# Performance work log

Hardware: AMD Instinct MI355X
Metric: run time of the kernel (lower is better)

Reference implementation:

```python
import jax, jax.numpy as jnp
import numpy as np

D_MODEL = 1024
NHEAD = 16
D_K = D_MODEL // NHEAD
D_CHUNK = 128


def setup_inputs() -> dict:
    key = jax.random.key(0)
    ks = jax.random.split(key, 11)
    B, S = 4, 8192
    s = 1.0 / np.sqrt(D_MODEL)
    inp = {
        "q": jax.random.normal(ks[0], (B, S, D_MODEL), jnp.float32),
        "k": jax.random.normal(ks[1], (B, S, D_MODEL), jnp.float32),
        "v": jax.random.normal(ks[2], (B, S, D_MODEL), jnp.float32),
        "W_Q": jax.random.normal(ks[3], (D_MODEL, D_MODEL), jnp.float32) * s,
        "b_Q": jnp.zeros((D_MODEL,), jnp.float32),
        "W_K": jax.random.normal(ks[4], (D_MODEL, D_MODEL), jnp.float32) * s,
        "b_K": jnp.zeros((D_MODEL,), jnp.float32),
        "W_V": jax.random.normal(ks[5], (D_MODEL, D_MODEL), jnp.float32) * s,
        "b_V": jnp.zeros((D_MODEL,), jnp.float32),
        "W_O": jax.random.normal(ks[6], (D_MODEL, D_MODEL), jnp.float32) * s,
        "b_O": jnp.zeros((D_MODEL,), jnp.float32),
    }
    return inp


def reference(q, k, v, W_Q, b_Q, W_K, b_K, W_V, b_V, W_O, b_O):
    B, S, _ = q.shape
    C = S // D_CHUNK  # number of chunks

    def split_heads(x):
        # [B,S,D] -> [B,H,C,P,dk]  (matches view+transpose+view in torch)
        x = x.reshape(B, S, NHEAD, D_K).transpose(0, 2, 1, 3)
        return x.reshape(B, NHEAD, C, D_CHUNK, D_K)

    Q = split_heads(q @ W_Q.T + b_Q)
    K = split_heads(k @ W_K.T + b_K)
    V = split_heads(v @ W_V.T + b_V)

    # block-diagonal local attention: each [P,P] score matrix per (b,h,chunk)
    scores = jnp.einsum("bhcpd,bhcqd->bhcpq", Q, K) / np.sqrt(D_K).astype(jnp.float32)
    attn_w = jax.nn.softmax(scores, axis=-1)
    attn = jnp.einsum("bhcpq,bhcqd->bhcpd", attn_w, V)  # [B,H,C,P,dk]

    # Faithful to torch: attn.transpose(1,2).view(B,-1,d_model)
    # i.e. flatten [C,H,P,dk] contiguously into rows of d_model.
    concat = attn.transpose(0, 2, 1, 3, 4).reshape(B, S, D_MODEL)
    return concat @ W_O.T + b_O
```

## Files before the change

kernel.cpp:

```cpp
#include <hip/hip_runtime.h>
#include <hip/hip_bf16.h>


typedef __attribute__((ext_vector_type(8))) short short8;
typedef __attribute__((ext_vector_type(4))) float f32x4;
typedef __attribute__((ext_vector_type(4))) unsigned short us4;
typedef __attribute__((ext_vector_type(4))) unsigned int u32x4;
typedef __attribute__((ext_vector_type(2))) unsigned int u32x2;

__device__ __forceinline__ unsigned short f2bf(float f) {
  unsigned u = __float_as_uint(f);
  u += 0x7fffu + ((u >> 16) & 1u);
  return (unsigned short)(u >> 16);
}

__device__ __forceinline__ unsigned cvtpk(float lo, float hi) {
  unsigned r;
  asm("v_cvt_pk_bf16_f32 %0, %1, %2" : "=v"(r) : "v"(lo), "v"(hi));
  return r;
}

__device__ __forceinline__ void gload16(const void* g, void* l) {
  __builtin_amdgcn_global_load_lds((const __attribute__((address_space(1))) void*)g,
                                   (__attribute__((address_space(3))) void*)l, 16, 0, 0);
}

__global__ void f2b4_kernel(const float* __restrict__ i0, const float* __restrict__ i1,
                            const float* __restrict__ i2, const float* __restrict__ i3,
                            unsigned short* __restrict__ o0, unsigned short* __restrict__ o1,
                            unsigned short* __restrict__ o2, unsigned short* __restrict__ o3,
                            int n) {
  const int z = blockIdx.z;
  const float* in = z == 0 ? i0 : z == 1 ? i1 : z == 2 ? i2 : i3;
  unsigned short* out = z == 0 ? o0 : z == 1 ? o1 : z == 2 ? o2 : o3;
  int i = (blockIdx.x * 256 + threadIdx.x) * 4;
  if (i >= n) return;
  f32x4 x = *(const f32x4*)(in + i);
  u32x2 o;
  o[0] = cvtpk(x[0], x[1]);
  o[1] = cvtpk(x[2], x[3]);
  *(u32x2*)(out + i) = o;
}

template<bool A_F32, bool C_F32>
__device__ __forceinline__ void gemm_core(const void* __restrict__ Apv,
                                          const unsigned short* __restrict__ Bp,
                                          const float* __restrict__ bias,
                                          void* __restrict__ Cp) {
  constexpr int BK = 64, NT = 16;
  const int tid = threadIdx.x;
  const int lane = tid & 63, wave = tid >> 6;
  const int lg = lane >> 4, li = lane & 15;
  const int wr = wave >> 2, wc = wave & 3;

  const unsigned short* Ab = (const unsigned short*)Apv;
  const float* Af = (const float*)Apv;

  const int orig = blockIdx.y * 4 + blockIdx.x;
  const int wg = (orig & 7) * 64 + (orig >> 3);
  const int bn = wg & 3, bm = wg >> 2;

  const long arow0 = (long)bm * 256;
  const int bcol0 = bn * 256;

  __shared__ __align__(16) unsigned short As[2][256 * BK];
  __shared__ __align__(16) unsigned short Bs[2][256 * BK];

  float bv[4];
  #pragma unroll
  for (int n = 0; n < 4; ++n) bv[n] = bias[bcol0 + wc * 64 + n * 16 + li];

  f32x4 acc[8][4];
  #pragma unroll
  for (int m = 0; m < 8; ++m)
    #pragma unroll
    for (int n = 0; n < 4; ++n) acc[m][n] = (f32x4){0.f, 0.f, 0.f, 0.f};

  auto stage_half = [&](int u, int h) {
    const int k0 = u * BK;
    const int half = h & 1;
    unsigned short* dst = (h < 2 ? As[u & 1] : Bs[u & 1]) + half * (128 * BK);
    const unsigned short* src = (h < 2) ? Ab : Bp;
    const long rbase = (h < 2) ? (arow0 + half * 128) : (long)(bcol0 + half * 128);
    #pragma unroll
    for (int it = 0; it < 2; ++it) {
      int s = it * 512 + tid;
      int row = s >> 3;
      int eg = ((s & 7) ^ (row & 7)) * 8;
      gload16(src + (rbase + row) * 1024 + k0 + eg, (unsigned char*)dst + s * 16);
    }
  };

  f32x4 areg[4][2];
  auto issueA = [&](int u) {
    #pragma unroll
    for (int hf = 0; hf < 2; ++hf)
      #pragma unroll
      for (int it = 0; it < 2; ++it) {
        int s = it * 512 + tid;
        int row = s >> 3;
        int ce = ((s & 7) ^ (row & 7)) * 8;
        const float* p = Af + (arow0 + hf * 128 + row) * 1024 + u * BK + ce;
        areg[hf * 2 + it][0] = *(const f32x4*)p;
        areg[hf * 2 + it][1] = *(const f32x4*)(p + 4);
      }
  };
  auto writeA_half = [&](int u, int hf) {
    unsigned short* dstb = As[u & 1] + hf * (128 * BK);
    #pragma unroll
    for (int it = 0; it < 2; ++it) {
      int s = it * 512 + tid;
      u32x4 o;
      o[0] = cvtpk(areg[hf * 2 + it][0][0], areg[hf * 2 + it][0][1]);
      o[1] = cvtpk(areg[hf * 2 + it][0][2], areg[hf * 2 + it][0][3]);
      o[2] = cvtpk(areg[hf * 2 + it][1][0], areg[hf * 2 + it][1][1]);
      o[3] = cvtpk(areg[hf * 2 + it][1][2], areg[hf * 2 + it][1][3]);
      *(u32x4*)((unsigned char*)dstb + s * 16) = o;
    }
  };

  if constexpr (A_F32) {
    stage_half(0, 2); stage_half(0, 3);
    issueA(0);
    stage_half(1, 2); stage_half(1, 3);
    writeA_half(0, 0); writeA_half(0, 1);
    asm volatile("s_waitcnt lgkmcnt(0)" ::: "memory");
    __builtin_amdgcn_sched_barrier(0);
    __builtin_amdgcn_s_barrier();
  } else {
    stage_half(0, 0); stage_half(0, 1); stage_half(0, 2); stage_half(0, 3);
    stage_half(1, 2); stage_half(1, 3);
    asm volatile("s_waitcnt vmcnt(4)" ::: "memory");
    __builtin_amdgcn_sched_barrier(0);
    __builtin_amdgcn_s_barrier();
  }

  for (int t = 0; t < NT; ++t) {
    const unsigned short* Asb = As[t & 1];
    const unsigned short* Bsb = Bs[t & 1];

    auto LDA = [&](int m, int kk) {
      return *(const short8*)(Asb + (wr * 128 + m * 16 + li) * BK +
                              (((kk * 4 + lg) ^ (li & 7)) * 8));
    };
    auto LDB = [&](int n, int kk) {
      return *(const short8*)(Bsb + (wc * 64 + n * 16 + li) * BK +
                              (((kk * 4 + lg) ^ (li & 7)) * 8));
    };

    short8 b0[4], b1[4];

    {
      short8 a0[4];
      #pragma unroll
      for (int i = 0; i < 4; ++i) a0[i] = LDA(i, 0);
      #pragma unroll
      for (int n = 0; n < 4; ++n) b0[n] = LDB(n, 0);
      if constexpr (A_F32) {
        if (t + 1 < NT) issueA(t + 1);
      } else {
        if (t + 1 < NT) stage_half(t + 1, 0);
      }
      __builtin_amdgcn_s_barrier();
      __builtin_amdgcn_s_setprio(1);
      #pragma unroll
      for (int i = 0; i < 4; ++i)
        #pragma unroll
        for (int n = 0; n < 4; ++n)
          acc[i][n] = __builtin_amdgcn_mfma_f32_16x16x32_bf16(a0[i], b0[n], acc[i][n], 0, 0, 0);
      __builtin_amdgcn_s_setprio(0);
      __builtin_amdgcn_s_barrier();
    }
    {
      short8 a1[4];
      #pragma unroll
      for (int i = 0; i < 4; ++i) a1[i] = LDA(i, 1);
      #pragma unroll
      for (int n = 0; n < 4; ++n) b1[n] = LDB(n, 1);
      if constexpr (!A_F32) {
        if (t + 1 < NT) stage_half(t + 1, 1);
      }
      __builtin_amdgcn_s_barrier();
      __builtin_amdgcn_s_setprio(1);
      #pragma unroll
      for (int i = 0; i < 4; ++i)
        #pragma unroll
        for (int n = 0; n < 4; ++n)
          acc[i][n] = __builtin_amdgcn_mfma_f32_16x16x32_bf16(a1[i], b1[n], acc[i][n], 0, 0, 0);
      __builtin_amdgcn_s_setprio(0);
      __builtin_amdgcn_s_barrier();
    }
    {
      short8 a2[4];
      #pragma unroll
      for (int i = 0; i < 4; ++i) a2[i] = LDA(4 + i, 0);
      if (t + 2 < NT) stage_half(t + 2, 2);
      __builtin_amdgcn_s_barrier();
      __builtin_amdgcn_s_setprio(1);
      #pragma unroll
      for (int i = 0; i < 4; ++i)
        #pragma unroll
        for (int n = 0; n < 4; ++n)
          acc[4 + i][n] = __builtin_amdgcn_mfma_f32_16x16x32_bf16(a2[i], b0[n], acc[4 + i][n], 0, 0, 0);
      if constexpr (A_F32) {
        if (t + 1 < NT) writeA_half(t + 1, 0);
      }
      __builtin_amdgcn_s_setprio(0);
      __builtin_amdgcn_s_barrier();
    }
    {
      short8 a3[4];
      #pragma unroll
      for (int i = 0; i < 4; ++i) a3[i] = LDA(4 + i, 1);
      if (t + 2 < NT) stage_half(t + 2, 3);
      if constexpr (!A_F32) {
        if (t + 2 < NT) {
          asm volatile("s_waitcnt vmcnt(4)" ::: "memory");
        } else {
          asm volatile("s_waitcnt vmcnt(0)" ::: "memory");
        }
        __builtin_amdgcn_sched_barrier(0);
      }
      __builtin_amdgcn_s_barrier();
      __builtin_amdgcn_s_setprio(1);
      #pragma unroll
      for (int i = 0; i < 4; ++i)
        #pragma unroll
        for (int n = 0; n < 4; ++n)
          acc[4 + i][n] = __builtin_amdgcn_mfma_f32_16x16x32_bf16(a3[i], b1[n], acc[4 + i][n], 0, 0, 0);
      if constexpr (A_F32) {
        if (t + 1 < NT) writeA_half(t + 1, 1);
        asm volatile("s_waitcnt lgkmcnt(0)" ::: "memory");
        __builtin_amdgcn_sched_barrier(0);
      }
      __builtin_amdgcn_s_setprio(0);
      __builtin_amdgcn_s_barrier();
    }
  }

  float* wsc = (float*)As + wave * (16 * 68);
  #pragma unroll
  for (int m = 0; m < 8; ++m) {
    #pragma unroll
    for (int n = 0; n < 4; ++n)
      #pragma unroll
      for (int r = 0; r < 4; ++r)
        wsc[(lg * 4 + r) * 68 + n * 16 + li] = acc[m][n][r] + bv[n];
    asm volatile("s_waitcnt lgkmcnt(0)" ::: "memory");
    __builtin_amdgcn_sched_barrier(0);
    #pragma unroll
    for (int i = 0; i < 4; ++i) {
      int slot = i * 64 + lane;
      int r = slot >> 4, g = slot & 15;
      f32x4 vv = *(const f32x4*)(wsc + r * 68 + g * 4);
      long grow = arow0 + wr * 128 + m * 16 + r;
      long gcol = bcol0 + wc * 64 + g * 4;
      if constexpr (C_F32) {
        *(f32x4*)((float*)Cp + grow * 1024 + gcol) = vv;
      } else {
        u32x2 o;
        o[0] = cvtpk(vv[0], vv[1]);
        o[1] = cvtpk(vv[2], vv[3]);
        *(u32x2*)((unsigned short*)Cp + grow * 1024 + gcol) = o;
      }
    }
    asm volatile("s_waitcnt lgkmcnt(0)" ::: "memory");
    __builtin_amdgcn_sched_barrier(0);
  }
}

__global__ __launch_bounds__(512, 2)
void gemm_proj(const float* __restrict__ A0, const float* __restrict__ A1,
               const float* __restrict__ A2,
               const unsigned short* __restrict__ B0, const unsigned short* __restrict__ B1,
               const unsigned short* __restrict__ B2,
               const float* __restrict__ b0, const float* __restrict__ b1,
               const float* __restrict__ b2,
               unsigned short* __restrict__ C0, unsigned short* __restrict__ C1,
               unsigned short* __restrict__ C2) {
  const int z = blockIdx.z;
  const float* Ap          = z == 0 ? A0 : z == 1 ? A1 : A2;
  const unsigned short* Bp = z == 0 ? B0 : z == 1 ? B1 : B2;
  const float* bias        = z == 0 ? b0 : z == 1 ? b1 : b2;
  unsigned short* Cp       = z == 0 ? C0 : z == 1 ? C1 : C2;
  gemm_core<true, false>(Ap, Bp, bias, Cp);
}

__global__ __launch_bounds__(512, 2)
void gemm_out(const unsigned short* __restrict__ Ap, const unsigned short* __restrict__ Bp,
              const float* __restrict__ bias, float* __restrict__ Cp) {
  gemm_core<false, true>(Ap, Bp, bias, Cp);
}

__global__ __launch_bounds__(256)
void attn_kernel(const unsigned short* __restrict__ Qp, const unsigned short* __restrict__ Kp,
                 const unsigned short* __restrict__ Vp, unsigned short* __restrict__ Cc) {
  const int bid = blockIdx.x;
  const int c = bid & 63, h = (bid >> 6) & 15, b = bid >> 10;
  const int tid = threadIdx.x;
  const int lane = tid & 63, wave = tid >> 6;
  const int lg = lane >> 4, li = lane & 15;

  __shared__ __align__(16) unsigned short Qs[128 * 64];
  __shared__ __align__(16) unsigned short Ks[128 * 64];
  __shared__ __align__(16) unsigned short Vs[128 * 64];
  __shared__ __align__(16) unsigned short Ps[4][32 * 128];

  const long base = ((long)(b * 8192 + c * 128)) * 1024 + h * 64;
  #pragma unroll
  for (int it = 0; it < 4; ++it) {
    int slot = it * 256 + tid;
    int row = slot >> 3;
    int colsw = ((slot & 7) ^ (row & 7)) * 8;
    int collin = (slot & 7) * 8;
    gload16(Qp + base + (long)row * 1024 + colsw, (unsigned char*)Qs + slot * 16);
    gload16(Kp + base + (long)row * 1024 + colsw, (unsigned char*)Ks + slot * 16);
    gload16(Vp + base + (long)row * 1024 + collin, (unsigned char*)Vs + slot * 16);
  }
  __syncthreads();

  f32x4 sc[2][8];
  #pragma unroll
  for (int m = 0; m < 2; ++m)
    #pragma unroll
    for (int n = 0; n < 8; ++n) sc[m][n] = (f32x4){0.f, 0.f, 0.f, 0.f};

  short8 qf[2][2];
  #pragma unroll
  for (int m = 0; m < 2; ++m)
    #pragma unroll
    for (int ks = 0; ks < 2; ++ks)
      qf[m][ks] = *(const short8*)(Qs + (wave * 32 + m * 16 + li) * 64 +
                                   (((ks * 4 + lg) ^ (li & 7)) * 8));

  #pragma unroll
  for (int n = 0; n < 8; ++n) {
    short8 kf0 = *(const short8*)(Ks + (n * 16 + li) * 64 + ((lg ^ (li & 7)) * 8));
    short8 kf1 = *(const short8*)(Ks + (n * 16 + li) * 64 + (((4 + lg) ^ (li & 7)) * 8));
    #pragma unroll
    for (int m = 0; m < 2; ++m) {
      sc[m][n] = __builtin_amdgcn_mfma_f32_16x16x32_bf16(qf[m][0], kf0, sc[m][n], 0, 0, 0);
      sc[m][n] = __builtin_amdgcn_mfma_f32_16x16x32_bf16(qf[m][1], kf1, sc[m][n], 0, 0, 0);
    }
  }

  #pragma unroll
  for (int m = 0; m < 2; ++m)
    #pragma unroll
    for (int r = 0; r < 4; ++r) {
      float mx = sc[m][0][r];
      #pragma unroll
      for (int n = 1; n < 8; ++n) mx = fmaxf(mx, sc[m][n][r]);
      #pragma unroll
      for (int d = 1; d < 16; d <<= 1) mx = fmaxf(mx, __shfl_xor(mx, d));
      float sum = 0.f;
      #pragma unroll
      for (int n = 0; n < 8; ++n) {
        float p = __expf((sc[m][n][r] - mx) * 0.125f);
        sc[m][n][r] = p;
        sum += p;
      }
      #pragma unroll
      for (int d = 1; d < 16; d <<= 1) sum += __shfl_xor(sum, d);
      float rinv = 1.f / sum;
      #pragma unroll
      for (int n = 0; n < 8; ++n) sc[m][n][r] *= rinv;
    }

  #pragma unroll
  for (int m = 0; m < 2; ++m)
    #pragma unroll
    for (int n = 0; n < 8; ++n)
      #pragma unroll
      for (int r = 0; r < 4; ++r) {
        int row = m * 16 + lg * 4 + r;
        int col = n * 16 + li;
        Ps[wave][row * 128 + (((col >> 3) ^ (row & 7)) * 8) + (col & 7)] = f2bf(sc[m][n][r]);
      }
  __syncthreads();

  f32x4 oc[2][4];
  #pragma unroll
  for (int m = 0; m < 2; ++m)
    #pragma unroll
    for (int n = 0; n < 4; ++n) oc[m][n] = (f32x4){0.f, 0.f, 0.f, 0.f};

  #pragma unroll
  for (int ks = 0; ks < 4; ++ks) {
    short8 vf[4];
    #pragma unroll
    for (int n = 0; n < 4; ++n)
      #pragma unroll
      for (int j = 0; j < 8; ++j)
        vf[n][j] = (short)Vs[(ks * 32 + lg * 8 + j) * 64 + n * 16 + li];
    #pragma unroll
    for (int m = 0; m < 2; ++m) {
      short8 pf = *(const short8*)(Ps[wave] + (m * 16 + li) * 128 +
                                   (((ks * 4 + lg) ^ (li & 7)) * 8));
      #pragma unroll
      for (int n = 0; n < 4; ++n)
        oc[m][n] = __builtin_amdgcn_mfma_f32_16x16x32_bf16(pf, vf[n], oc[m][n], 0, 0, 0);
    }
  }

  #pragma unroll
  for (int m = 0; m < 2; ++m)
    #pragma unroll
    for (int n = 0; n < 4; ++n)
      #pragma unroll
      for (int r = 0; r < 4; ++r) {
        int p = wave * 32 + m * 16 + lg * 4 + r;
        int d = n * 16 + li;
        int s = c * 128 + h * 8 + (p >> 4);
        int colo = (p & 15) * 64 + d;
        Cc[((long)(b * 8192 + s)) * 1024 + colo] = f2bf(oc[m][n][r]);
      }
}

extern "C" void kernel_launch(void* const* d_in, const int* in_sizes, int n_in,
                              void* d_out, int out_size, void* d_ws, size_t ws_size,
                              hipStream_t stream) {
  (void)in_sizes; (void)n_in; (void)out_size; (void)ws_size;
  const float* q  = (const float*)d_in[0];
  const float* k  = (const float*)d_in[1];
  const float* v  = (const float*)d_in[2];
  const float* WQ = (const float*)d_in[3];
  const float* bQ = (const float*)d_in[4];
  const float* WK = (const float*)d_in[5];
  const float* bK = (const float*)d_in[6];
  const float* WV = (const float*)d_in[7];
  const float* bV = (const float*)d_in[8];
  const float* WO = (const float*)d_in[9];
  const float* bO = (const float*)d_in[10];

  const size_t MN = 32768ull * 1024ull;
  unsigned short* Qp  = (unsigned short*)d_ws;
  unsigned short* Kp  = Qp + MN;
  unsigned short* Vp  = Kp + MN;
  unsigned short* Cc  = Vp + MN;
  unsigned short* WQb = Cc + MN;
  unsigned short* WKb = WQb + (1 << 20);
  unsigned short* WVb = WKb + (1 << 20);
  unsigned short* WOb = WVb + (1 << 20);

  dim3 gw(1024, 1, 4);
  f2b4_kernel<<<gw, 256, 0, stream>>>(WQ, WK, WV, WO, WQb, WKb, WVb, WOb, 1 << 20);

  dim3 gp(4, 128, 3);
  gemm_proj<<<gp, 512, 0, stream>>>(q, k, v, WQb, WKb, WVb, bQ, bK, bV, Qp, Kp, Vp);

  attn_kernel<<<4096, 256, 0, stream>>>(Qp, Kp, Vp, Cc);

  dim3 go(4, 128);
  gemm_out<<<go, 512, 0, stream>>>(Cc, WOb, bO, (float*)d_out);
}
```

Baseline: 514.2 us.

## Prefetch fp32 A tiles two steps ahead with ping-pong register buffers

For the fp32-A GEMM path, the global loads of the A tile are now issued two k-iterations ahead instead of one, using two alternating register buffers (even and odd). The main loop is unrolled by two so the buffers swap roles statically, and explicit vmcnt waits gate the convert-and-write to LDS. The aim is to hide more global-load latency for the fp32 activations. In exchange it doubles the A staging registers, which risks lower occupancy or spills, and the loop assumes NT is even.

```diff
diff --git a/kernel.cpp b/kernel.cpp
--- a/kernel.cpp
+++ b/kernel.cpp
@@ -91,8 +91,8 @@
     }
   };
 
-  f32x4 areg[4][2];
-  auto issueA = [&](int u) {
+  f32x4 aregE[4][2], aregO[4][2];
+  auto issueA = [&](int u, f32x4 (&ar)[4][2]) {
     #pragma unroll
     for (int hf = 0; hf < 2; ++hf)
       #pragma unroll
@@ -101,29 +101,143 @@
         int row = s >> 3;
         int ce = ((s & 7) ^ (row & 7)) * 8;
         const float* p = Af + (arow0 + hf * 128 + row) * 1024 + u * BK + ce;
-        areg[hf * 2 + it][0] = *(const f32x4*)p;
-        areg[hf * 2 + it][1] = *(const f32x4*)(p + 4);
+        ar[hf * 2 + it][0] = *(const f32x4*)p;
+        ar[hf * 2 + it][1] = *(const f32x4*)(p + 4);
       }
   };
-  auto writeA_half = [&](int u, int hf) {
+  auto writeAh = [&](int u, int hf, f32x4 (&ar)[4][2]) {
     unsigned short* dstb = As[u & 1] + hf * (128 * BK);
     #pragma unroll
     for (int it = 0; it < 2; ++it) {
       int s = it * 512 + tid;
       u32x4 o;
-      o[0] = cvtpk(areg[hf * 2 + it][0][0], areg[hf * 2 + it][0][1]);
-      o[1] = cvtpk(areg[hf * 2 + it][0][2], areg[hf * 2 + it][0][3]);
-      o[2] = cvtpk(areg[hf * 2 + it][1][0], areg[hf * 2 + it][1][1]);
-      o[3] = cvtpk(areg[hf * 2 + it][1][2], areg[hf * 2 + it][1][3]);
+      o[0] = cvtpk(ar[hf * 2 + it][0][0], ar[hf * 2 + it][0][1]);
+      o[1] = cvtpk(ar[hf * 2 + it][0][2], ar[hf * 2 + it][0][3]);
+      o[2] = cvtpk(ar[hf * 2 + it][1][0], ar[hf * 2 + it][1][1]);
+      o[3] = cvtpk(ar[hf * 2 + it][1][2], ar[hf * 2 + it][1][3]);
       *(u32x4*)((unsigned char*)dstb + s * 16) = o;
     }
   };
 
+  auto tile_body = [&](int t, f32x4 (&arI)[4][2], f32x4 (&arW)[4][2]) {
+    const unsigned short* Asb = As[t & 1];
+    const unsigned short* Bsb = Bs[t & 1];
+
+    auto LDA = [&](int m, int kk) {
+      return *(const short8*)(Asb + (wr * 128 + m * 16 + li) * BK +
+                              (((kk * 4 + lg) ^ (li & 7)) * 8));
+    };
+    auto LDB = [&](int n, int kk) {
+      return *(const short8*)(Bsb + (wc * 64 + n * 16 + li) * BK +
+                              (((kk * 4 + lg) ^ (li & 7)) * 8));
+    };
+
+    short8 b0[4], b1[4];
+
+    {
+      short8 a0[4];
+      #pragma unroll
+      for (int i = 0; i < 4; ++i) a0[i] = LDA(i, 0);
+      #pragma unroll
+      for (int n = 0; n < 4; ++n) b0[n] = LDB(n, 0);
+      if constexpr (A_F32) {
+        if (t + 2 < NT) issueA(t + 2, arI);
+      } else {
+        if (t + 1 < NT) stage_half(t + 1, 0);
+      }
+      __builtin_amdgcn_s_barrier();
+      __builtin_amdgcn_s_setprio(1);
+      #pragma unroll
+      for (int i = 0; i < 4; ++i)
+        #pragma unroll
+        for (int n = 0; n < 4; ++n)
+          acc[i][n] = __builtin_amdgcn_mfma_f32_16x16x32_bf16(a0[i], b0[n], acc[i][n], 0, 0, 0);
+      __builtin_amdgcn_s_setprio(0);
+      __builtin_amdgcn_s_barrier();
+    }
+    {
+      short8 a1[4];
+      #pragma unroll
+      for (int i = 0; i < 4; ++i) a1[i] = LDA(i, 1);
+      #pragma unroll
+      for (int n = 0; n < 4; ++n) b1[n] = LDB(n, 1);
+      if constexpr (!A_F32) {
+        if (t + 1 < NT) stage_half(t + 1, 1);
+      }
+      __builtin_amdgcn_s_barrier();
+      __builtin_amdgcn_s_setprio(1);
+      #pragma unroll
+      for (int i = 0; i < 4; ++i)
+        #pragma unroll
+        for (int n = 0; n < 4; ++n)
+          acc[i][n] = __builtin_amdgcn_mfma_f32_16x16x32_bf16(a1[i], b1[n], acc[i][n], 0, 0, 0);
+      __builtin_amdgcn_s_setprio(0);
+      __builtin_amdgcn_s_barrier();
+    }
+    {
+      short8 a2[4];
+      #pragma unroll
+      for (int i = 0; i < 4; ++i) a2[i] = LDA(4 + i, 0);
+      if (t + 2 < NT) stage_half(t + 2, 2);
+      __builtin_amdgcn_s_barrier();
+      __builtin_amdgcn_s_setprio(1);
+      #pragma unroll
+      for (int i = 0; i < 4; ++i)
+        #pragma unroll
+        for (int n = 0; n < 4; ++n)
+          acc[4 + i][n] = __builtin_amdgcn_mfma_f32_16x16x32_bf16(a2[i], b0[n], acc[4 + i][n], 0, 0, 0);
+      if constexpr (A_F32) {
+        if (t + 1 < NT) writeAh(t + 1, 0, arW);
+      }
+      __builtin_amdgcn_s_setprio(0);
+      __builtin_amdgcn_s_barrier();
+    }
+    {
+      short8 a3[4];
+      #pragma unroll
+      for (int i = 0; i < 4; ++i) a3[i] = LDA(4 + i, 1);
+      if (t + 2 < NT) stage_half(t + 2, 3);
+      if constexpr (!A_F32) {
+        if (t + 2 < NT) {
+          asm volatile("s_waitcnt vmcnt(4)" ::: "memory");
+        } else {
+          asm volatile("s_waitcnt vmcnt(0)" ::: "memory");
+        }
+        __builtin_amdgcn_sched_barrier(0);
+      }
+      __builtin_amdgcn_s_barrier();
+      __builtin_amdgcn_s_setprio(1);
+      #pragma unroll
+      for (int i = 0; i < 4; ++i)
+        #pragma unroll
+        for (int n = 0; n < 4; ++n)
+          acc[4 + i][n] = __builtin_amdgcn_mfma_f32_16x16x32_bf16(a3[i], b1[n], acc[4 + i][n], 0, 0, 0);
+      if constexpr (A_F32) {
+        if (t + 1 < NT) {
+          writeAh(t + 1, 1, arW);
+          if (t + 2 < NT) {
+            asm volatile("s_waitcnt vmcnt(12)" ::: "memory");
+          } else {
+            asm volatile("s_waitcnt vmcnt(0)" ::: "memory");
+          }
+          __builtin_amdgcn_sched_barrier(0);
+          asm volatile("s_waitcnt lgkmcnt(0)" ::: "memory");
+          __builtin_amdgcn_sched_barrier(0);
+        }
+      }
+      __builtin_amdgcn_s_setprio(0);
+      __builtin_amdgcn_s_barrier();
+    }
+  };
+
   if constexpr (A_F32) {
+    issueA(0, aregE);
     stage_half(0, 2); stage_half(0, 3);
-    issueA(0);
+    issueA(1, aregO);
     stage_half(1, 2); stage_half(1, 3);
-    writeA_half(0, 0); writeA_half(0, 1);
+    writeAh(0, 0, aregE); writeAh(0, 1, aregE);
+    asm volatile("s_waitcnt vmcnt(12)" ::: "memory");
+    __builtin_amdgcn_sched_barrier(0);
     asm volatile("s_waitcnt lgkmcnt(0)" ::: "memory");
     __builtin_amdgcn_sched_barrier(0);
     __builtin_amdgcn_s_barrier();
@@ -135,107 +249,10 @@
     __builtin_amdgcn_s_barrier();
   }
 
-  for (int t = 0; t < NT; ++t) {
-    const unsigned short* Asb = As[t & 1];
-    const unsigned short* Bsb = Bs[t & 1];
-
-    auto LDA = [&](int m, int kk) {
-      return *(const short8*)(Asb + (wr * 128 + m * 16 + li) * BK +
-                              (((kk * 4 + lg) ^ (li & 7)) * 8));
-    };
-    auto LDB = [&](int n, int kk) {
-      return *(const short8*)(Bsb + (wc * 64 + n * 16 + li) * BK +
-                              (((kk * 4 + lg) ^ (li & 7)) * 8));
-    };
-
-    short8 b0[4], b1[4];
-
-    {
-      short8 a0[4];
-      #pragma unroll
-      for (int i = 0; i < 4; ++i) a0[i] = LDA(i, 0);
-      #pragma unroll
-      for (int n = 0; n < 4; ++n) b0[n] = LDB(n, 0);
-      if constexpr (A_F32) {
-        if (t + 1 < NT) issueA(t + 1);
-      } else {
-        if (t + 1 < NT) stage_half(t + 1, 0);
-      }
-      __builtin_amdgcn_s_barrier();
-      __builtin_amdgcn_s_setprio(1);
-      #pragma unroll
-      for (int i = 0; i < 4; ++i)
-        #pragma unroll
-        for (int n = 0; n < 4; ++n)
-          acc[i][n] = __builtin_amdgcn_mfma_f32_16x16x32_bf16(a0[i], b0[n], acc[i][n], 0, 0, 0);
-      __builtin_amdgcn_s_setprio(0);
-      __builtin_amdgcn_s_barrier();
-    }
-    {
-      short8 a1[4];
-      #pragma unroll
-      for (int i = 0; i < 4; ++i) a1[i] = LDA(i, 1);
-      #pragma unroll
-      for (int n = 0; n < 4; ++n) b1[n] = LDB(n, 1);
-      if constexpr (!A_F32) {
-        if (t + 1 < NT) stage_half(t + 1, 1);
-      }
-      __builtin_amdgcn_s_barrier();
-      __builtin_amdgcn_s_setprio(1);
-      #pragma unroll
-      for (int i = 0; i < 4; ++i)
-        #pragma unroll
-        for (int n = 0; n < 4; ++n)
-          acc[i][n] = __builtin_amdgcn_mfma_f32_16x16x32_bf16(a1[i], b1[n], acc[i][n], 0, 0, 0);
-      __builtin_amdgcn_s_setprio(0);
-      __builtin_amdgcn_s_barrier();
-    }
-    {
-      short8 a2[4];
-      #pragma unroll
-      for (int i = 0; i < 4; ++i) a2[i] = LDA(4 + i, 0);
-      if (t + 2 < NT) stage_half(t + 2, 2);
-      __builtin_amdgcn_s_barrier();
-      __builtin_amdgcn_s_setprio(1);
-      #pragma unroll
-      for (int i = 0; i < 4; ++i)
-        #pragma unroll
-        for (int n = 0; n < 4; ++n)
-          acc[4 + i][n] = __builtin_amdgcn_mfma_f32_16x16x32_bf16(a2[i], b0[n], acc[4 + i][n], 0, 0, 0);
-      if constexpr (A_F32) {
-        if (t + 1 < NT) writeA_half(t + 1, 0);
-      }
-      __builtin_amdgcn_s_setprio(0);
-      __builtin_amdgcn_s_barrier();
-    }
-    {
-      short8 a3[4];
-      #pragma unroll
-      for (int i = 0; i < 4; ++i) a3[i] = LDA(4 + i, 1);
-      if (t + 2 < NT) stage_half(t + 2, 3);
-      if constexpr (!A_F32) {
-        if (t + 2 < NT) {
-          asm volatile("s_waitcnt vmcnt(4)" ::: "memory");
-        } else {
-          asm volatile("s_waitcnt vmcnt(0)" ::: "memory");
-        }
-        __builtin_amdgcn_sched_barrier(0);
-      }
-      __builtin_amdgcn_s_barrier();
-      __builtin_amdgcn_s_setprio(1);
-      #pragma unroll
-      for (int i = 0; i < 4; ++i)
-        #pragma unroll
-        for (int n = 0; n < 4; ++n)
-          acc[4 + i][n] = __builtin_amdgcn_mfma_f32_16x16x32_bf16(a3[i], b1[n], acc[4 + i][n], 0, 0, 0);
-      if constexpr (A_F32) {
-        if (t + 1 < NT) writeA_half(t + 1, 1);
-        asm volatile("s_waitcnt lgkmcnt(0)" ::: "memory");
-        __builtin_amdgcn_sched_barrier(0);
-      }
-      __builtin_amdgcn_s_setprio(0);
-      __builtin_amdgcn_s_barrier();
-    }
+  #pragma unroll 1
+  for (int tt = 0; tt < NT; tt += 2) {
+    tile_body(tt,     aregE, aregO);
+    tile_body(tt + 1, aregO, aregE);
   }
 
   float* wsc = (float*)As + wave * (16 * 68);
```

New measurement: 887.7 us. 1.73x slower.
